# Performance work log

Hardware: AMD Instinct MI355X
Metric: run time of the kernel (lower is better)

Reference implementation:

```python
import jax, jax.numpy as jnp
import numpy as np

NEG_SLOPE = 0.01  # torch nn.LeakyReLU default

B, N, IN_F, OUT_F, HEADS = 4, 2048, 512, 512, 8
D = OUT_F // HEADS  # 64


def setup_inputs() -> dict:
    key = jax.random.key(0)
    ks = jax.random.split(key, 4)
    X = jax.random.normal(ks[0], (B, N, IN_F), dtype=jnp.float32)
    W_v = jax.random.normal(ks[1], (IN_F, D), dtype=jnp.float32) * (IN_F ** -0.5)
    b_v = jnp.zeros((D,), dtype=jnp.float32)
    W_q = jax.random.normal(ks[2], (D, HEADS), dtype=jnp.float32) * (D ** -0.5)
    b_q = jnp.zeros((HEADS,), dtype=jnp.float32)
    W_k = jax.random.normal(ks[3], (D, HEADS), dtype=jnp.float32) * (D ** -0.5)
    b_k = jnp.zeros((HEADS,), dtype=jnp.float32)
    return {"X": X, "W_v": W_v, "b_v": b_v, "W_q": W_q, "b_q": b_q, "W_k": W_k, "b_k": b_k}


def reference(X, W_v, b_v, W_q, b_q, W_k, b_k):
    # V: (B, N, D)
    V = X @ W_v + b_v
    # per-node, per-head scalar scores: (B, N, H) -> (B, H, N)
    Q = jnp.swapaxes(V @ W_q + b_q, 1, 2)
    K = jnp.swapaxes(V @ W_k + b_k, 1, 2)
    # A[b,h,i,j] = leaky_relu(Q[b,h,j] + K[b,h,i])  (broadcast outer-sum)
    A = jax.nn.leaky_relu(Q[:, :, None, :] + K[:, :, :, None], negative_slope=NEG_SLOPE)
    A = jax.nn.softmax(A, axis=-1)  # dropout = identity in eval mode
    # H[b,i,h,f] = sum_j A[b,h,i,j] V[b,j,f]
    H = jnp.einsum('bhij,bjf->bihf', A, V)
    return H.reshape(H.shape[0], H.shape[1], -1)  # (B, N, H*D)
```

## Files before the change

kernel.cpp:

```cpp
#include <hip/hip_runtime.h>

#define BB   4
#define NN   2048
#define INF  512
#define HH   8
#define DD   64
#define BH   (BB*HH)
#define NCK  16
#define CKS  128
#define KSP  8


__global__ __launch_bounds__(256) void k_vpart(
    const float* __restrict__ X, const float* __restrict__ Wv,
    float* __restrict__ Vpart)
{
  const int t   = threadIdx.x;
  const int d   = t & 63;
  const int wid = __builtin_amdgcn_readfirstlane(blockIdx.x * 4 + (t >> 6));
  const int rg  = wid >> 3;
  const int ks  = wid & 7;
  const int k0  = ks * 64;
  float wreg[64];
  const float* wp = Wv + (size_t)k0 * DD + d;
  #pragma unroll
  for (int kk = 0; kk < 64; kk++) wreg[kk] = wp[(size_t)kk * DD];
  const float* xp = X + (size_t)(rg * 16) * INF + k0;
  float* vp = Vpart + ((size_t)ks * (BB*NN) + (size_t)rg * 16) * DD + d;
  for (int r = 0; r < 16; r++) {
    float a0 = 0.f, a1 = 0.f, a2 = 0.f, a3 = 0.f;
    #pragma unroll
    for (int kk = 0; kk < 64; kk += 4) {
      a0 += xp[kk+0] * wreg[kk+0];
      a1 += xp[kk+1] * wreg[kk+1];
      a2 += xp[kk+2] * wreg[kk+2];
      a3 += xp[kk+3] * wreg[kk+3];
    }
    vp[(size_t)r * DD] = (a0 + a1) + (a2 + a3);
    xp += INF;
  }
}

__global__ __launch_bounds__(256) void k_vred(
    const float* __restrict__ Vpart, const float* __restrict__ bv,
    const float* __restrict__ Wq, const float* __restrict__ bq,
    const float* __restrict__ Wk, const float* __restrict__ bk,
    float* __restrict__ V, float* __restrict__ qsg, float* __restrict__ ksg)
{
  __shared__ float Vs[16][DD + 1];
  const int t  = threadIdx.x;
  const size_t e0 = ((size_t)blockIdx.x * 256 + t) * 4;
  const size_t STR = (size_t)BB * NN * DD;
  float4 a = *(const float4*)(Vpart + e0);
  #pragma unroll
  for (int p = 1; p < KSP; p++) {
    const float4 b = *(const float4*)(Vpart + (size_t)p * STR + e0);
    a.x += b.x;  a.y += b.y;  a.z += b.z;  a.w += b.w;
  }
  const float4 bb = *(const float4*)(bv + (e0 & 63));
  a.x += bb.x;  a.y += bb.y;  a.z += bb.z;  a.w += bb.w;
  *(float4*)(V + e0) = a;
  const int lrow = t >> 4;
  const int lcol = (t * 4) & 63;
  Vs[lrow][lcol]   = a.x;  Vs[lrow][lcol+1] = a.y;
  Vs[lrow][lcol+2] = a.z;  Vs[lrow][lcol+3] = a.w;
  __syncthreads();
  const int row = t >> 4;
  const int h   = t & 7;
  const bool isK = (t & 8) != 0;
  const float* W = isK ? Wk : Wq;
  float s = isK ? bk[h] : bq[h];
  #pragma unroll 8
  for (int dd = 0; dd < DD; dd++) s += Vs[row][dd] * W[dd*HH + h];
  const int grow = blockIdx.x * 16 + row;
  const int b = grow >> 11, n = grow & (NN - 1);
  (isK ? ksg : qsg)[(b*HH + h) * NN + n] = s;
}

__global__ __launch_bounds__(1024) void k_sort(
    float* __restrict__ q, unsigned short* __restrict__ idxg)
{
  __shared__ float key[NN];
  __shared__ int   idx[NN];
  const int t  = threadIdx.x;
  const int bh = blockIdx.x;
  key[t]        = q[bh*NN + t];        idx[t]        = t;
  key[t + 1024] = q[bh*NN + t + 1024]; idx[t + 1024] = t + 1024;
  __syncthreads();

#define CEX_STAGE(size, stride)                                         \
  {                                                                     \
    const int i = ((t & ~((stride) - 1)) << 1) | (t & ((stride) - 1));  \
    const int j = i + (stride);                                         \
    const bool up = ((i & (size)) == 0);                                \
    const float a = key[i], b = key[j];                                 \
    if (up ? (a > b) : (a < b)) {                                       \
      key[i] = b; key[j] = a;                                           \
      const int tmp = idx[i]; idx[i] = idx[j]; idx[j] = tmp;            \
    }                                                                   \
  }

  for (int size = 2; size <= 128; size <<= 1)
    for (int stride = size >> 1; stride > 0; stride >>= 1)
      CEX_STAGE(size, stride)
  __syncthreads();
  for (int size = 256; size <= 2048; size <<= 1) {
    for (int stride = size >> 1; stride >= 128; stride >>= 1) {
      CEX_STAGE(size, stride)
      __syncthreads();
    }
    for (int stride = 64; stride > 0; stride >>= 1)
      CEX_STAGE(size, stride)
    __syncthreads();
  }
#undef CEX_STAGE

  q[bh*NN + t]        = key[t];
  q[bh*NN + t + 1024] = key[t + 1024];
  idxg[bh*NN + t]        = (unsigned short)idx[t];
  idxg[bh*NN + t + 1024] = (unsigned short)idx[t + 1024];
}

__global__ __launch_bounds__(256) void k_scan(
    const float* __restrict__ sq, const unsigned short* __restrict__ idxg,
    const float* __restrict__ V,
    float* __restrict__ P1, float* __restrict__ P2,
    float* __restrict__ l1, float* __restrict__ l2,
    float* __restrict__ S1g, float* __restrict__ S2g,
    float* __restrict__ SL1, float* __restrict__ SL2)
{
  __shared__ float ss1[4][64], ss2[4][64], sl1[4], sl2[4];
  const int t  = threadIdx.x;
  const int bh = blockIdx.x >> 4;
  const int ck = blockIdx.x & 15;
  const int d  = t & 63, g = t >> 6;
  const int r0 = ck*CKS + g*32;
  const float* Vb  = V + (size_t)(bh >> 3) * NN * DD;
  const float* sqb = sq + bh*NN;
  const unsigned short* ib = idxg + bh*NN;
  float a1 = 0.f, a2 = 0.f, s1 = 0.f, s2 = 0.f;
  #pragma unroll 8
  for (int rr = 0; rr < 32; rr++) {
    const int r = r0 + rr;
    const float qv = sqb[r];
    const float e1 = __expf(qv), e2 = __expf(0.01f*qv);
    const float v  = Vb[(size_t)ib[r]*DD + d];
    a1 += e1*v;  a2 += e2*v;  s1 += e1;  s2 += e2;
  }
  ss1[g][d] = a1;  ss2[g][d] = a2;
  if (d == 0) { sl1[g] = s1;  sl2[g] = s2; }
  __syncthreads();
  float o1 = 0.f, o2 = 0.f, lo1 = 0.f, lo2 = 0.f;
  for (int gg = 0; gg < g; gg++) { o1 += ss1[gg][d]; o2 += ss2[gg][d]; lo1 += sl1[gg]; lo2 += sl2[gg]; }
  if (g == 0) {
    S1g[(bh*NCK + ck)*64 + d] = ss1[0][d]+ss1[1][d]+ss1[2][d]+ss1[3][d];
    S2g[(bh*NCK + ck)*64 + d] = ss2[0][d]+ss2[1][d]+ss2[2][d]+ss2[3][d];
    if (d == 0) {
      SL1[bh*NCK + ck] = sl1[0]+sl1[1]+sl1[2]+sl1[3];
      SL2[bh*NCK + ck] = sl2[0]+sl2[1]+sl2[2]+sl2[3];
    }
  }
  a1 = o1; a2 = o2; s1 = lo1; s2 = lo2;
  float* P1b = P1 + (size_t)bh*NN*DD;
  float* P2b = P2 + (size_t)bh*NN*DD;
  #pragma unroll 8
  for (int rr = 0; rr < 32; rr++) {
    const int r = r0 + rr;
    const float qv = sqb[r];
    const float e1 = __expf(qv), e2 = __expf(0.01f*qv);
    const float v  = Vb[(size_t)ib[r]*DD + d];
    P1b[(size_t)r*DD + d] = a1;
    P2b[(size_t)r*DD + d] = a2;
    if (d == 0) { l1[bh*NN + r] = s1;  l2[bh*NN + r] = s2; }
    a1 += e1*v;  a2 += e2*v;  s1 += e1;  s2 += e2;
  }
}

__global__ __launch_bounds__(256) void k_off(
    const float* __restrict__ S1g, const float* __restrict__ S2g,
    const float* __restrict__ SL1, const float* __restrict__ SL2,
    float* __restrict__ Off1, float* __restrict__ Off2,
    float* __restrict__ Loff1, float* __restrict__ Loff2)
{
  const int bh = blockIdx.x;
  const int t  = threadIdx.x;
  if (t < 128) {
    const int d = t & 63;
    const bool h2 = t >= 64;
    const float* S = h2 ? S2g : S1g;
    float* O = h2 ? Off2 : Off1;
    double a = 0.0;
    for (int ck = 0; ck < NCK; ck++) {
      O[((size_t)bh*(NCK+1) + ck)*64 + d] = (float)a;
      a += (double)S[((size_t)bh*NCK + ck)*64 + d];
    }
    O[((size_t)bh*(NCK+1) + NCK)*64 + d] = (float)a;
  } else if (t == 128 || t == 129) {
    const bool h2 = (t == 129);
    const float* S = h2 ? SL2 : SL1;
    float* O = h2 ? Loff2 : Loff1;
    double a = 0.0;
    for (int ck = 0; ck < NCK; ck++) { O[bh*(NCK+1) + ck] = (float)a; a += (double)S[bh*NCK + ck]; }
    O[bh*(NCK+1) + NCK] = (float)a;
  }
}

__global__ __launch_bounds__(256) void k_out(
    const float* __restrict__ sq, const float* __restrict__ ksg,
    const float* __restrict__ P1, const float* __restrict__ P2,
    const float* __restrict__ Off1, const float* __restrict__ Off2,
    const float* __restrict__ l1, const float* __restrict__ l2,
    const float* __restrict__ Loff1, const float* __restrict__ Loff2,
    float* __restrict__ out)
{
  const int t  = threadIdx.x;
  const int bh = blockIdx.x >> 9;
  const int i  = ((blockIdx.x & 511) << 2) + (t >> 6);
  const int d  = t & 63;
  const int b  = bh >> 3, h = bh & 7;
  const float kv = ksg[bh*NN + i];
  const float tt = -kv;
  const float* s = sq + bh*NN;
  const unsigned long long m1 = __ballot(s[d*32 + 31] <= tt);
  const int c1 = __popcll(m1);
  int pos;
  if (c1 == 64) pos = NN;
  else {
    const int bs = c1 << 5;
    const unsigned long long m2 = __ballot(s[bs + (d & 31)] <= tt);
    pos = bs + (__popcll(m2) >> 1);
  }
  const float ek  = __expf(kv);
  const float ek2 = __expf(0.01f * kv);
  const size_t base = (size_t)bh * NN * DD;
  const float T1  = Off1[((size_t)bh*(NCK+1) + NCK)*64 + d];
  const float Lt1 = Loff1[bh*(NCK+1) + NCK];
  float p1v, p2v, q1v, q2v;
  if (pos < NN) {
    const int ch = pos >> 7;
    p1v = P1[base + (size_t)pos*DD + d] + Off1[((size_t)bh*(NCK+1) + ch)*64 + d];
    p2v = P2[base + (size_t)pos*DD + d] + Off2[((size_t)bh*(NCK+1) + ch)*64 + d];
    q1v = l1[bh*NN + pos] + Loff1[bh*(NCK+1) + ch];
    q2v = l2[bh*NN + pos] + Loff2[bh*(NCK+1) + ch];
  } else {
    p1v = T1;   p2v = Off2[((size_t)bh*(NCK+1) + NCK)*64 + d];
    q1v = Lt1;  q2v = Loff2[bh*(NCK+1) + NCK];
  }
  const float num = ek * (T1 - p1v)  + ek2 * p2v;
  const float den = ek * (Lt1 - q1v) + ek2 * q2v;
  out[((size_t)(b*NN + i)) * (HH*DD) + h*DD + d] = num / den;
}

extern "C" void kernel_launch(void* const* d_in, const int* in_sizes, int n_in,
                              void* d_out, int out_size, void* d_ws, size_t ws_size,
                              hipStream_t stream)
{
  (void)in_sizes; (void)n_in; (void)out_size; (void)ws_size;
  const float* X  = (const float*)d_in[0];
  const float* Wv = (const float*)d_in[1];
  const float* bv = (const float*)d_in[2];
  const float* Wq = (const float*)d_in[3];
  const float* bq = (const float*)d_in[4];
  const float* Wk = (const float*)d_in[5];
  const float* bk = (const float*)d_in[6];
  float* out = (float*)d_out;

  float* w = (float*)d_ws;
  float* V     = w;  w += (size_t)BB*NN*DD;
  float* qsg   = w;  w += BH*NN;
  float* ksg   = w;  w += BH*NN;
  float* l1    = w;  w += BH*NN;
  float* l2    = w;  w += BH*NN;
  unsigned short* idxg = (unsigned short*)w;  w += BH*NN/2;
  float* Off1  = w;  w += BH*(NCK+1)*DD;
  float* Off2  = w;  w += BH*(NCK+1)*DD;
  float* Loff1 = w;  w += BH*(NCK+1);
  float* Loff2 = w;  w += BH*(NCK+1);
  float* P1    = w;  w += (size_t)BH*NN*DD;
  float* P2    = w;  w += (size_t)BH*NN*DD;

  float* Vpart = P1;

  float* S1g = out;
  float* S2g = S1g + BH*NCK*DD;
  float* SL1 = S2g + BH*NCK*DD;
  float* SL2 = SL1 + BH*NCK;

  k_vpart<<<1024, 256, 0, stream>>>(X, Wv, Vpart);
  k_vred <<<512, 256, 0, stream>>>(Vpart, bv, Wq, bq, Wk, bk, V, qsg, ksg);
  k_sort <<<BH, 1024, 0, stream>>>(qsg, idxg);
  k_scan <<<BH*NCK, 256, 0, stream>>>(qsg, idxg, V, P1, P2, l1, l2, S1g, S2g, SL1, SL2);
  k_off  <<<BH, 256, 0, stream>>>(S1g, S2g, SL1, SL2, Off1, Off2, Loff1, Loff2);
  k_out  <<<BH*512, 256, 0, stream>>>(qsg, ksg, P1, P2, Off1, Off2, l1, l2, Loff1, Loff2, out);
}
```

Baseline: 157.4 us.

## Tile X@Wv projection through shared memory with 4x4 register blocking

Replaces the per-wavefront register-held weight slice GEMV-style projection with a shared-memory tiled GEMM. Each 256-thread block stages 64x64 tiles of X and Wv in LDS and computes a 4x4 output micro-tile per thread. The K split drops from 8 to 4 partials, which halves the partial-sum traffic that k_vred must reduce. This raises arithmetic intensity and uses coalesced float4 loads, at the cost of LDS usage and block-wide syncs.

```diff
diff --git a/kernel.cpp b/kernel.cpp
--- a/kernel.cpp
+++ b/kernel.cpp
@@ -8,36 +8,53 @@
 #define BH   (BB*HH)
 #define NCK  16
 #define CKS  128
-#define KSP  8
-
-
-__global__ __launch_bounds__(256) void k_vpart(
+#define KSP  4
+
+
+__global__ __launch_bounds__(256) void k_v(
     const float* __restrict__ X, const float* __restrict__ Wv,
     float* __restrict__ Vpart)
 {
-  const int t   = threadIdx.x;
-  const int d   = t & 63;
-  const int wid = __builtin_amdgcn_readfirstlane(blockIdx.x * 4 + (t >> 6));
-  const int rg  = wid >> 3;
-  const int ks  = wid & 7;
-  const int k0  = ks * 64;
-  float wreg[64];
-  const float* wp = Wv + (size_t)k0 * DD + d;
+  __shared__ float Xs[64][68];
+  __shared__ float Ws[64][68];
+  const int t  = threadIdx.x;
+  const int tr = t >> 4;
+  const int tc = t & 15;
+  const int rg = blockIdx.x >> 2;
+  const int ks = blockIdx.x & 3;
+  const int r0 = rg * 64;
+  const int k0 = ks * 128;
+  float acc[4][4] = {{0.f}};
+
+  for (int kc = k0; kc < k0 + 128; kc += 64) {
+    __syncthreads();
+    #pragma unroll
+    for (int i = 0; i < 4; i++) {
+      const int e  = t + i * 256;
+      const int rw = e >> 4;
+      const int c4 = (e & 15) * 4;
+      *(float4*)(&Xs[rw][c4]) = *(const float4*)(X  + (size_t)(r0 + rw) * INF + kc + c4);
+      *(float4*)(&Ws[rw][c4]) = *(const float4*)(Wv + (size_t)(kc + rw) * DD  + c4);
+    }
+    __syncthreads();
+    #pragma unroll 8
+    for (int k = 0; k < 64; k++) {
+      const float4 w4 = *(const float4*)(&Ws[k][tc * 4]);
+      const float x0 = Xs[tr*4+0][k];
+      const float x1 = Xs[tr*4+1][k];
+      const float x2 = Xs[tr*4+2][k];
+      const float x3 = Xs[tr*4+3][k];
+      acc[0][0] += x0*w4.x; acc[0][1] += x0*w4.y; acc[0][2] += x0*w4.z; acc[0][3] += x0*w4.w;
+      acc[1][0] += x1*w4.x; acc[1][1] += x1*w4.y; acc[1][2] += x1*w4.z; acc[1][3] += x1*w4.w;
+      acc[2][0] += x2*w4.x; acc[2][1] += x2*w4.y; acc[2][2] += x2*w4.z; acc[2][3] += x2*w4.w;
+      acc[3][0] += x3*w4.x; acc[3][1] += x3*w4.y; acc[3][2] += x3*w4.z; acc[3][3] += x3*w4.w;
+    }
+  }
+  float* vp = Vpart + ((size_t)ks * (BB*NN) + r0) * DD;
   #pragma unroll
-  for (int kk = 0; kk < 64; kk++) wreg[kk] = wp[(size_t)kk * DD];
-  const float* xp = X + (size_t)(rg * 16) * INF + k0;
-  float* vp = Vpart + ((size_t)ks * (BB*NN) + (size_t)rg * 16) * DD + d;
-  for (int r = 0; r < 16; r++) {
-    float a0 = 0.f, a1 = 0.f, a2 = 0.f, a3 = 0.f;
-    #pragma unroll
-    for (int kk = 0; kk < 64; kk += 4) {
-      a0 += xp[kk+0] * wreg[kk+0];
-      a1 += xp[kk+1] * wreg[kk+1];
-      a2 += xp[kk+2] * wreg[kk+2];
-      a3 += xp[kk+3] * wreg[kk+3];
-    }
-    vp[(size_t)r * DD] = (a0 + a1) + (a2 + a3);
-    xp += INF;
+  for (int i = 0; i < 4; i++) {
+    float4 o;  o.x = acc[i][0];  o.y = acc[i][1];  o.z = acc[i][2];  o.w = acc[i][3];
+    *(float4*)(vp + (size_t)(4*tr + i) * DD + 4*tc) = o;
   }
 }
 
@@ -286,7 +303,7 @@
   float* SL1 = S2g + BH*NCK*DD;
   float* SL2 = SL1 + BH*NCK;
 
-  k_vpart<<<1024, 256, 0, stream>>>(X, Wv, Vpart);
+  k_v    <<<512, 256, 0, stream>>>(X, Wv, Vpart);
   k_vred <<<512, 256, 0, stream>>>(Vpart, bv, Wq, bq, Wk, bk, V, qsg, ksg);
   k_sort <<<BH, 1024, 0, stream>>>(qsg, idxg);
   k_scan <<<BH*NCK, 256, 0, stream>>>(qsg, idxg, V, P1, P2, l1, l2, S1g, S2g, SL1, SL2);
```

New measurement: 143.1 us. 1.1x faster.
